# Kernel optimization log

Measured on AMD Instinct MI355X. Metric: run time of the kernel, lower is better.

Reference implementation:

```python
import jax, jax.numpy as jnp
import numpy as np

B, T, F, H = 256, 128, 1024, 512  # batch, input_size (time window), feature_dim, hidden_size


def setup_inputs() -> dict:
    key = jax.random.key(0)
    ks = jax.random.split(key, 7)
    in1 = T + 2 * H
    return {
        "h": jax.random.normal(ks[0], (B, H), dtype=jnp.float32),
        "s": jax.random.normal(ks[1], (B, H), dtype=jnp.float32),
        "x": jax.random.normal(ks[2], (B, T, F), dtype=jnp.float32),
        "W1": jax.random.normal(ks[3], (T, in1), dtype=jnp.float32) / np.sqrt(in1),
        "b1": jnp.zeros((T,), dtype=jnp.float32),
        "W2": jax.random.normal(ks[4], (1, T), dtype=jnp.float32) / np.sqrt(T),
        "b2": jnp.zeros((1,), dtype=jnp.float32),
    }


def reference(h, s, x, W1, b1, W2, b2):
    feature_dim = x.shape[-1]
    xp = jnp.transpose(x, (2, 0, 1))                     # [F, B, T]
    hb = jnp.broadcast_to(h[None], (feature_dim,) + h.shape)  # [F, B, H]
    sb = jnp.broadcast_to(s[None], (feature_dim,) + s.shape)  # [F, B, H]
    cat = jnp.concatenate([xp, hb, sb], axis=-1)         # [F, B, T+2H]
    u = jnp.einsum('fbk,tk->fbt', cat, W1) + b1          # [F, B, T]
    e = jnp.einsum('fbt,ot->fbo', jnp.tanh(u), W2) + b2  # [F, B, 1]
    alpha = jax.nn.softmax(e, axis=0)[..., 0]            # softmax over feature dim -> [F, B]
    return alpha.T                                       # [B, F]
```

## Files before the change

### kernel.cpp

```cpp
#include <hip/hip_runtime.h>
#include <hip/hip_bf16.h>


#define B_N 256
#define T_N 128
#define F_N 1024
#define H_N 512
#define IN1 1152

typedef __bf16 bf16x8 __attribute__((ext_vector_type(8)));
typedef float f32x16 __attribute__((ext_vector_type(16)));
typedef float f32x4_t __attribute__((ext_vector_type(4)));

__device__ __forceinline__ float wave_reduce_sum(float v) {
#pragma unroll
  for (int off = 32; off >= 1; off >>= 1) v += __shfl_xor(v, off, 64);
  return v;
}
__device__ __forceinline__ float wave_reduce_max(float v) {
#pragma unroll
  for (int off = 32; off >= 1; off >>= 1) v = fmaxf(v, __shfl_xor(v, off, 64));
  return v;
}

__device__ __forceinline__ float tanh_fast(float u) {
  u = fminf(fmaxf(u, -15.f), 15.f);
  float e2 = __expf(2.f * u);
  return (e2 - 1.f) / (e2 + 1.f);
}

#define HSP 1028
__global__ __launch_bounds__(256) void kA_c(const float* __restrict__ h,
                                            const float* __restrict__ s,
                                            const float* __restrict__ W1,
                                            const float* __restrict__ b1,
                                            float* __restrict__ c) {
  __shared__ __align__(16) float hs[8 * HSP];
  int tid = threadIdx.x;
  int bg = blockIdx.x >> 2;
  int tg = blockIdx.x & 3;
#pragma unroll
  for (int i = 0; i < 8; ++i) {
    int p = tid + 256 * i;
    int bl = p >> 8;
    int j4 = p & 255;
    int b = bg * 8 + bl;
    float4 v;
    if (j4 < 128) v = reinterpret_cast<const float4*>(h + (size_t)b * H_N)[j4];
    else v = reinterpret_cast<const float4*>(s + (size_t)b * H_N)[j4 - 128];
    *reinterpret_cast<float4*>(&hs[bl * HSP + j4 * 4]) = v;
  }
  __syncthreads();
  int bl = tid >> 5, ti = tid & 31;
  int t = tg * 32 + ti;
  int b = bg * 8 + bl;
  const float4* wrow = reinterpret_cast<const float4*>(W1 + (size_t)t * IN1 + T_N);
  const float4* vrow = reinterpret_cast<const float4*>(&hs[bl * HSP]);
  float acc = 0.f;
#pragma unroll 4
  for (int j4 = 0; j4 < 256; ++j4) {
    float4 w = wrow[j4], v = vrow[j4];
    acc += w.x * v.x + w.y * v.y + w.z * v.z + w.w * v.w;
  }
  c[b * T_N + t] = acc + b1[t];
}

__global__ __launch_bounds__(256) void kA_frag(const float* __restrict__ W1,
                                               unsigned short* __restrict__ w1frag) {
  int i = blockIdx.x * 256 + threadIdx.x;
  int p0 = i * 2;
  int j = p0 & 7;
  int lane = (p0 >> 3) & 63;
  int kk = (p0 >> 9) & 7;
  int tt = (p0 >> 12) & 3;
  int t = tt * 32 + (lane & 31);
  int k = kk * 16 + 8 * (lane >> 5) + j;
  const float2 w = *reinterpret_cast<const float2*>(W1 + t * IN1 + k);
  __bf16 a = (__bf16)w.x, bq = (__bf16)w.y;
  unsigned short ua = __builtin_bit_cast(unsigned short, a);
  unsigned short ub = __builtin_bit_cast(unsigned short, bq);
  *reinterpret_cast<unsigned*>(w1frag + p0) = (unsigned)ua | ((unsigned)ub << 16);
}

__global__ __launch_bounds__(256) void kB_e(const float* __restrict__ x,
                                            const unsigned short* __restrict__ w1frag,
                                            const float* __restrict__ c,
                                            const float* __restrict__ W2,
                                            const float* __restrict__ b2,
                                            float* __restrict__ e) {
  __shared__ __align__(16) unsigned short w1lds[16384];
  __shared__ __align__(16) float clds[T_N];
  __shared__ __align__(16) float w2lds[T_N];
  __shared__ __align__(16) float epart[4][T_N];
  int tid = threadIdx.x;
  int b = blockIdx.x >> 3;
  int fg = blockIdx.x & 7;

  {
    const uint4* src = reinterpret_cast<const uint4*>(w1frag);
    uint4* dst = reinterpret_cast<uint4*>(w1lds);
#pragma unroll
    for (int i = 0; i < 8; ++i) dst[tid + 256 * i] = src[tid + 256 * i];
  }
  if (tid < T_N) clds[tid] = c[b * T_N + tid];
  else if (tid < 2 * T_N) w2lds[tid - T_N] = W2[tid - T_N];
  __syncthreads();

  int lane = tid & 63, wave = tid >> 6;
  int g = lane >> 5, l31 = lane & 31;
  int f0 = fg * 128;

  const float4* xb4 = reinterpret_cast<const float4*>(x + (size_t)b * T_N * F_N + f0);
  const bf16x8* af = reinterpret_cast<const bf16x8*>(w1lds);

  f32x16 acc0 = {}, acc1 = {}, acc2 = {}, acc3 = {};
#pragma unroll
  for (int kk = 0; kk < 8; ++kk) {
    float4 xq[8];
#pragma unroll
    for (int j = 0; j < 8; ++j)
      xq[j] = xb4[(size_t)(kk * 16 + 8 * g + j) * 256 + l31];
    bf16x8 bf0, bf1, bf2, bf3;
#pragma unroll
    for (int j = 0; j < 8; ++j) {
      bf0[j] = (__bf16)xq[j].x;
      bf1[j] = (__bf16)xq[j].y;
      bf2[j] = (__bf16)xq[j].z;
      bf3[j] = (__bf16)xq[j].w;
    }
    bf16x8 afr = af[wave * 512 + kk * 64 + lane];
    acc0 = __builtin_amdgcn_mfma_f32_32x32x16_bf16(afr, bf0, acc0, 0, 0, 0);
    acc1 = __builtin_amdgcn_mfma_f32_32x32x16_bf16(afr, bf1, acc1, 0, 0, 0);
    acc2 = __builtin_amdgcn_mfma_f32_32x32x16_bf16(afr, bf2, acc2, 0, 0, 0);
    acc3 = __builtin_amdgcn_mfma_f32_32x32x16_bf16(afr, bf3, acc3, 0, 0, 0);
  }

  int tbase = wave * 32 + 4 * g;
  float4 es = {0.f, 0.f, 0.f, 0.f};
#pragma unroll
  for (int q = 0; q < 4; ++q) {
    f32x4_t cq = *reinterpret_cast<const f32x4_t*>(&clds[tbase + 8 * q]);
    f32x4_t wq = *reinterpret_cast<const f32x4_t*>(&w2lds[tbase + 8 * q]);
#pragma unroll
    for (int r = 0; r < 4; ++r) {
      int reg = q * 4 + r;
      float w2v = wq[r], cv = cq[r];
      es.x += w2v * tanh_fast(acc0[reg] + cv);
      es.y += w2v * tanh_fast(acc1[reg] + cv);
      es.z += w2v * tanh_fast(acc2[reg] + cv);
      es.w += w2v * tanh_fast(acc3[reg] + cv);
    }
  }
  es.x += __shfl_xor(es.x, 32, 64);
  es.y += __shfl_xor(es.y, 32, 64);
  es.z += __shfl_xor(es.z, 32, 64);
  es.w += __shfl_xor(es.w, 32, 64);
  if (g == 0) *reinterpret_cast<float4*>(&epart[wave][4 * l31]) = es;
  __syncthreads();
  if (tid < T_N) {
    float sum = epart[0][tid] + epart[1][tid] + epart[2][tid] + epart[3][tid] + b2[0];
    e[(size_t)b * F_N + f0 + tid] = sum;
  }
}

__global__ __launch_bounds__(256) void kC_softmax(float* __restrict__ out) {
  int b = blockIdx.x, tid = threadIdx.x;
  int lane = tid & 63, wid = tid >> 6;
  float* row = out + (size_t)b * F_N;
  float v[4];
#pragma unroll
  for (int q = 0; q < 4; ++q) v[q] = row[tid + 256 * q];
  float m = fmaxf(fmaxf(v[0], v[1]), fmaxf(v[2], v[3]));
  m = wave_reduce_max(m);
  __shared__ float rm[4], rs[4];
  if (lane == 0) rm[wid] = m;
  __syncthreads();
  float M = fmaxf(fmaxf(rm[0], rm[1]), fmaxf(rm[2], rm[3]));
  float ssum = 0.f;
#pragma unroll
  for (int q = 0; q < 4; ++q) {
    v[q] = __expf(v[q] - M);
    ssum += v[q];
  }
  ssum = wave_reduce_sum(ssum);
  if (lane == 0) rs[wid] = ssum;
  __syncthreads();
  float S = rs[0] + rs[1] + rs[2] + rs[3];
  float inv = 1.f / S;
#pragma unroll
  for (int q = 0; q < 4; ++q) row[tid + 256 * q] = v[q] * inv;
}

extern "C" void kernel_launch(void* const* d_in, const int* in_sizes, int n_in,
                              void* d_out, int out_size, void* d_ws, size_t ws_size,
                              hipStream_t stream) {
  const float* h = (const float*)d_in[0];
  const float* s = (const float*)d_in[1];
  const float* x = (const float*)d_in[2];
  const float* W1 = (const float*)d_in[3];
  const float* b1 = (const float*)d_in[4];
  const float* W2 = (const float*)d_in[5];
  const float* b2 = (const float*)d_in[6];
  float* out = (float*)d_out;

  float* c_ws = (float*)d_ws;
  unsigned short* w1frag = (unsigned short*)((char*)d_ws + B_N * T_N * 4);

  kA_c<<<128, 256, 0, stream>>>(h, s, W1, b1, c_ws);
  kA_frag<<<32, 256, 0, stream>>>(W1, w1frag);
  kB_e<<<2048, 256, 0, stream>>>(x, w1frag, c_ws, W2, b2, out);
  kC_softmax<<<256, 256, 0, stream>>>(out);
}
```

Before: 250.4 us.

## Fuse all four kernels into one per-batch block kernel

Replaces the separate c-projection, W1 fragment packing, MFMA score and softmax kernels with one kernel where each 1024-thread block handles one batch row. Each block computes its own c vector and bf16 W1 fragments in LDS, loops over four feature passes for the MFMA/tanh scoring, then does the softmax in LDS. This removes three launches and the global round-trips of c, w1frag and e. In exchange it recomputes W1 packing per block and reduces the grid to one block per batch, with narrower x loads and barriers between passes.

```diff
diff --git a/kernel.cpp b/kernel.cpp
--- a/kernel.cpp
+++ b/kernel.cpp
@@ -22,173 +22,152 @@
   for (int off = 32; off >= 1; off >>= 1) v = fmaxf(v, __shfl_xor(v, off, 64));
   return v;
 }
-
 __device__ __forceinline__ float tanh_fast(float u) {
   u = fminf(fmaxf(u, -15.f), 15.f);
   float e2 = __expf(2.f * u);
   return (e2 - 1.f) / (e2 + 1.f);
 }
+__device__ __forceinline__ unsigned short bfbits(float f) {
+  return __builtin_bit_cast(unsigned short, (__bf16)f);
+}
 
-#define HSP 1028
-__global__ __launch_bounds__(256) void kA_c(const float* __restrict__ h,
-                                            const float* __restrict__ s,
-                                            const float* __restrict__ W1,
-                                            const float* __restrict__ b1,
-                                            float* __restrict__ c) {
-  __shared__ __align__(16) float hs[8 * HSP];
-  int tid = threadIdx.x;
-  int bg = blockIdx.x >> 2;
-  int tg = blockIdx.x & 3;
+__global__ __launch_bounds__(1024) void kFused(const float* __restrict__ h,
+                                               const float* __restrict__ s,
+                                               const float* __restrict__ x,
+                                               const float* __restrict__ W1,
+                                               const float* __restrict__ b1,
+                                               const float* __restrict__ W2,
+                                               const float* __restrict__ b2,
+                                               float* __restrict__ out) {
+  __shared__ __align__(16) unsigned short w1frag[16384];
+  __shared__ __align__(16) float hs[1024];
+  __shared__ __align__(16) float cpart[128][8];
+  __shared__ __align__(16) float clds[T_N];
+  __shared__ __align__(16) float w2lds[T_N];
+  __shared__ __align__(16) float epart[4][256];
+  __shared__ __align__(16) float elds[F_N];
+  __shared__ float rbuf[16];
+
+  const int tid = threadIdx.x;
+  const int b = blockIdx.x;
+
+  if (tid < 256) {
+    float4 v = (tid < 128) ? reinterpret_cast<const float4*>(h + (size_t)b * H_N)[tid]
+                           : reinterpret_cast<const float4*>(s + (size_t)b * H_N)[tid - 128];
+    reinterpret_cast<float4*>(hs)[tid] = v;
+  }
+  {
+    const int kk = (tid >> 5) & 7;
+    const int tt = tid >> 8;
 #pragma unroll
-  for (int i = 0; i < 8; ++i) {
-    int p = tid + 256 * i;
-    int bl = p >> 8;
-    int j4 = p & 255;
-    int b = bg * 8 + bl;
-    float4 v;
-    if (j4 < 128) v = reinterpret_cast<const float4*>(h + (size_t)b * H_N)[j4];
-    else v = reinterpret_cast<const float4*>(s + (size_t)b * H_N)[j4 - 128];
-    *reinterpret_cast<float4*>(&hs[bl * HSP + j4 * 4]) = v;
+    for (int sub = 0; sub < 2; ++sub) {
+      int lane = ((tid << 1) + sub) & 63;
+      int t = tt * 32 + (lane & 31);
+      int k0 = kk * 16 + 8 * (lane >> 5);
+      const float4* wsrc = reinterpret_cast<const float4*>(W1 + (size_t)t * IN1 + k0);
+      float4 w0 = wsrc[0], w1v = wsrc[1];
+      uint4 pk;
+      pk.x = (unsigned)bfbits(w0.x) | ((unsigned)bfbits(w0.y) << 16);
+      pk.y = (unsigned)bfbits(w0.z) | ((unsigned)bfbits(w0.w) << 16);
+      pk.z = (unsigned)bfbits(w1v.x) | ((unsigned)bfbits(w1v.y) << 16);
+      pk.w = (unsigned)bfbits(w1v.z) | ((unsigned)bfbits(w1v.w) << 16);
+      *reinterpret_cast<uint4*>(w1frag + ((size_t)((tt * 8 + kk) * 64 + lane) * 8)) = pk;
+    }
   }
   __syncthreads();
-  int bl = tid >> 5, ti = tid & 31;
-  int t = tg * 32 + ti;
-  int b = bg * 8 + bl;
-  const float4* wrow = reinterpret_cast<const float4*>(W1 + (size_t)t * IN1 + T_N);
-  const float4* vrow = reinterpret_cast<const float4*>(&hs[bl * HSP]);
-  float acc = 0.f;
-#pragma unroll 4
-  for (int j4 = 0; j4 < 256; ++j4) {
-    float4 w = wrow[j4], v = vrow[j4];
-    acc += w.x * v.x + w.y * v.y + w.z * v.z + w.w * v.w;
-  }
-  c[b * T_N + t] = acc + b1[t];
-}
-
-__global__ __launch_bounds__(256) void kA_frag(const float* __restrict__ W1,
-                                               unsigned short* __restrict__ w1frag) {
-  int i = blockIdx.x * 256 + threadIdx.x;
-  int p0 = i * 2;
-  int j = p0 & 7;
-  int lane = (p0 >> 3) & 63;
-  int kk = (p0 >> 9) & 7;
-  int tt = (p0 >> 12) & 3;
-  int t = tt * 32 + (lane & 31);
-  int k = kk * 16 + 8 * (lane >> 5) + j;
-  const float2 w = *reinterpret_cast<const float2*>(W1 + t * IN1 + k);
-  __bf16 a = (__bf16)w.x, bq = (__bf16)w.y;
-  unsigned short ua = __builtin_bit_cast(unsigned short, a);
-  unsigned short ub = __builtin_bit_cast(unsigned short, bq);
-  *reinterpret_cast<unsigned*>(w1frag + p0) = (unsigned)ua | ((unsigned)ub << 16);
-}
-
-__global__ __launch_bounds__(256) void kB_e(const float* __restrict__ x,
-                                            const unsigned short* __restrict__ w1frag,
-                                            const float* __restrict__ c,
-                                            const float* __restrict__ W2,
-                                            const float* __restrict__ b2,
-                                            float* __restrict__ e) {
-  __shared__ __align__(16) unsigned short w1lds[16384];
-  __shared__ __align__(16) float clds[T_N];
-  __shared__ __align__(16) float w2lds[T_N];
-  __shared__ __align__(16) float epart[4][T_N];
-  int tid = threadIdx.x;
-  int b = blockIdx.x >> 3;
-  int fg = blockIdx.x & 7;
 
   {
-    const uint4* src = reinterpret_cast<const uint4*>(w1frag);
-    uint4* dst = reinterpret_cast<uint4*>(w1lds);
+    const int t = tid >> 3, part = tid & 7;
+    const float4* wrow = reinterpret_cast<const float4*>(W1 + (size_t)t * IN1 + T_N + part * 128);
+    const float4* vrow = reinterpret_cast<const float4*>(hs + part * 128);
+    float acc = 0.f;
+#pragma unroll 4
+    for (int k4 = 0; k4 < 32; ++k4) {
+      float4 w = wrow[k4], v = vrow[k4];
+      acc += w.x * v.x + w.y * v.y + w.z * v.z + w.w * v.w;
+    }
+    cpart[t][part] = acc;
+  }
+  __syncthreads();
+  if (tid < 128) {
+    float cs = 0.f;
 #pragma unroll
-    for (int i = 0; i < 8; ++i) dst[tid + 256 * i] = src[tid + 256 * i];
+    for (int i = 0; i < 8; ++i) cs += cpart[tid][i];
+    clds[tid] = cs + b1[tid];
+  } else if (tid < 256) {
+    w2lds[tid - 128] = W2[tid - 128];
   }
-  if (tid < T_N) clds[tid] = c[b * T_N + tid];
-  else if (tid < 2 * T_N) w2lds[tid - T_N] = W2[tid - T_N];
   __syncthreads();
 
-  int lane = tid & 63, wave = tid >> 6;
-  int g = lane >> 5, l31 = lane & 31;
-  int f0 = fg * 128;
+  const int lane = tid & 63, wave = tid >> 6;
+  const int g = lane >> 5, l31 = lane & 31;
+  const int tt = wave & 3, fgrp = wave >> 2;
+  const bf16x8* af = reinterpret_cast<const bf16x8*>(w1frag);
+  const float b2v = b2[0];
 
-  const float4* xb4 = reinterpret_cast<const float4*>(x + (size_t)b * T_N * F_N + f0);
-  const bf16x8* af = reinterpret_cast<const bf16x8*>(w1lds);
-
-  f32x16 acc0 = {}, acc1 = {}, acc2 = {}, acc3 = {};
+  for (int pass = 0; pass < 4; ++pass) {
+    const int f0 = pass * 256 + fgrp * 64;
+    const float2* xb2 = reinterpret_cast<const float2*>(x + (size_t)b * T_N * F_N + f0);
+    f32x16 acc0 = {}, acc1 = {};
 #pragma unroll
-  for (int kk = 0; kk < 8; ++kk) {
-    float4 xq[8];
+    for (int kk = 0; kk < 8; ++kk) {
+      float2 xq[8];
 #pragma unroll
-    for (int j = 0; j < 8; ++j)
-      xq[j] = xb4[(size_t)(kk * 16 + 8 * g + j) * 256 + l31];
-    bf16x8 bf0, bf1, bf2, bf3;
+      for (int j = 0; j < 8; ++j)
+        xq[j] = xb2[(size_t)(kk * 16 + 8 * g + j) * 512 + l31];
+      bf16x8 bf0, bf1;
 #pragma unroll
-    for (int j = 0; j < 8; ++j) {
-      bf0[j] = (__bf16)xq[j].x;
-      bf1[j] = (__bf16)xq[j].y;
-      bf2[j] = (__bf16)xq[j].z;
-      bf3[j] = (__bf16)xq[j].w;
+      for (int j = 0; j < 8; ++j) {
+        bf0[j] = (__bf16)xq[j].x;
+        bf1[j] = (__bf16)xq[j].y;
+      }
+      bf16x8 afr = af[tt * 512 + kk * 64 + lane];
+      acc0 = __builtin_amdgcn_mfma_f32_32x32x16_bf16(afr, bf0, acc0, 0, 0, 0);
+      acc1 = __builtin_amdgcn_mfma_f32_32x32x16_bf16(afr, bf1, acc1, 0, 0, 0);
     }
-    bf16x8 afr = af[wave * 512 + kk * 64 + lane];
-    acc0 = __builtin_amdgcn_mfma_f32_32x32x16_bf16(afr, bf0, acc0, 0, 0, 0);
-    acc1 = __builtin_amdgcn_mfma_f32_32x32x16_bf16(afr, bf1, acc1, 0, 0, 0);
-    acc2 = __builtin_amdgcn_mfma_f32_32x32x16_bf16(afr, bf2, acc2, 0, 0, 0);
-    acc3 = __builtin_amdgcn_mfma_f32_32x32x16_bf16(afr, bf3, acc3, 0, 0, 0);
+    const int tbase = tt * 32 + 4 * g;
+    float ex = 0.f, ey = 0.f;
+#pragma unroll
+    for (int q = 0; q < 4; ++q) {
+      f32x4_t cq = *reinterpret_cast<const f32x4_t*>(&clds[tbase + 8 * q]);
+      f32x4_t wq = *reinterpret_cast<const f32x4_t*>(&w2lds[tbase + 8 * q]);
+#pragma unroll
+      for (int r = 0; r < 4; ++r) {
+        int reg = q * 4 + r;
+        ex += wq[r] * tanh_fast(acc0[reg] + cq[r]);
+        ey += wq[r] * tanh_fast(acc1[reg] + cq[r]);
+      }
+    }
+    ex += __shfl_xor(ex, 32, 64);
+    ey += __shfl_xor(ey, 32, 64);
+    if (g == 0) {
+      float2 e2v = {ex, ey};
+      *reinterpret_cast<float2*>(&epart[tt][fgrp * 64 + 2 * l31]) = e2v;
+    }
+    __syncthreads();
+    if (tid < 256) {
+      elds[pass * 256 + tid] =
+          epart[0][tid] + epart[1][tid] + epart[2][tid] + epart[3][tid] + b2v;
+    }
+    __syncthreads();
   }
 
-  int tbase = wave * 32 + 4 * g;
-  float4 es = {0.f, 0.f, 0.f, 0.f};
+  float v = elds[tid];
+  float m = wave_reduce_max(v);
+  if (lane == 0) rbuf[wave] = m;
+  __syncthreads();
+  float M = rbuf[0];
 #pragma unroll
-  for (int q = 0; q < 4; ++q) {
-    f32x4_t cq = *reinterpret_cast<const f32x4_t*>(&clds[tbase + 8 * q]);
-    f32x4_t wq = *reinterpret_cast<const f32x4_t*>(&w2lds[tbase + 8 * q]);
+  for (int i = 1; i < 16; ++i) M = fmaxf(M, rbuf[i]);
+  float ev = __expf(v - M);
+  float ssum = wave_reduce_sum(ev);
+  __syncthreads();
+  if (lane == 0) rbuf[wave] = ssum;
+  __syncthreads();
+  float S = 0.f;
 #pragma unroll
-    for (int r = 0; r < 4; ++r) {
-      int reg = q * 4 + r;
-      float w2v = wq[r], cv = cq[r];
-      es.x += w2v * tanh_fast(acc0[reg] + cv);
-      es.y += w2v * tanh_fast(acc1[reg] + cv);
-      es.z += w2v * tanh_fast(acc2[reg] + cv);
-      es.w += w2v * tanh_fast(acc3[reg] + cv);
-    }
-  }
-  es.x += __shfl_xor(es.x, 32, 64);
-  es.y += __shfl_xor(es.y, 32, 64);
-  es.z += __shfl_xor(es.z, 32, 64);
-  es.w += __shfl_xor(es.w, 32, 64);
-  if (g == 0) *reinterpret_cast<float4*>(&epart[wave][4 * l31]) = es;
-  __syncthreads();
-  if (tid < T_N) {
-    float sum = epart[0][tid] + epart[1][tid] + epart[2][tid] + epart[3][tid] + b2[0];
-    e[(size_t)b * F_N + f0 + tid] = sum;
-  }
-}
-
-__global__ __launch_bounds__(256) void kC_softmax(float* __restrict__ out) {
-  int b = blockIdx.x, tid = threadIdx.x;
-  int lane = tid & 63, wid = tid >> 6;
-  float* row = out + (size_t)b * F_N;
-  float v[4];
-#pragma unroll
-  for (int q = 0; q < 4; ++q) v[q] = row[tid + 256 * q];
-  float m = fmaxf(fmaxf(v[0], v[1]), fmaxf(v[2], v[3]));
-  m = wave_reduce_max(m);
-  __shared__ float rm[4], rs[4];
-  if (lane == 0) rm[wid] = m;
-  __syncthreads();
-  float M = fmaxf(fmaxf(rm[0], rm[1]), fmaxf(rm[2], rm[3]));
-  float ssum = 0.f;
-#pragma unroll
-  for (int q = 0; q < 4; ++q) {
-    v[q] = __expf(v[q] - M);
-    ssum += v[q];
-  }
-  ssum = wave_reduce_sum(ssum);
-  if (lane == 0) rs[wid] = ssum;
-  __syncthreads();
-  float S = rs[0] + rs[1] + rs[2] + rs[3];
-  float inv = 1.f / S;
-#pragma unroll
-  for (int q = 0; q < 4; ++q) row[tid + 256 * q] = v[q] * inv;
+  for (int i = 0; i < 16; ++i) S += rbuf[i];
+  out[(size_t)b * F_N + tid] = ev / S;
 }
 
 extern "C" void kernel_launch(void* const* d_in, const int* in_sizes, int n_in,
@@ -203,11 +182,5 @@
   const float* b2 = (const float*)d_in[6];
   float* out = (float*)d_out;
 
-  float* c_ws = (float*)d_ws;
-  unsigned short* w1frag = (unsigned short*)((char*)d_ws + B_N * T_N * 4);
-
-  kA_c<<<128, 256, 0, stream>>>(h, s, W1, b1, c_ws);
-  kA_frag<<<32, 256, 0, stream>>>(W1, w1frag);
-  kB_e<<<2048, 256, 0, stream>>>(x, w1frag, c_ws, W2, b2, out);
-  kC_softmax<<<256, 256, 0, stream>>>(out);
+  kFused<<<256, 1024, 0, stream>>>(h, s, x, W1, b1, W2, b2, out);
 }
```

After: 254.0 us. No clear change (+1.4%).

## Stage x tile as bf16 in LDS and restructure h/s projection kernel

Applied to the files above, without the earlier changes.

The main kernel now loads its x tile cooperatively with float2 reads across rows, converts it to bf16 once, and writes it to LDS in MFMA B-fragment order. The MFMA loop then reads B operands from LDS instead of issuing strided global float4 loads per wave. The c-projection kernel is rewritten so each block holds one W1 row in registers and uses wave reductions over batches, launched with twice as many blocks. The extra 32KB of LDS per block may lower occupancy in the main kernel.

```diff
diff --git a/kernel.cpp b/kernel.cpp
--- a/kernel.cpp
+++ b/kernel.cpp
@@ -11,6 +11,7 @@
 typedef __bf16 bf16x8 __attribute__((ext_vector_type(8)));
 typedef float f32x16 __attribute__((ext_vector_type(16)));
 typedef float f32x4_t __attribute__((ext_vector_type(4)));
+typedef unsigned int u32x4 __attribute__((ext_vector_type(4)));
 
 __device__ __forceinline__ float wave_reduce_sum(float v) {
 #pragma unroll
@@ -22,47 +23,39 @@
   for (int off = 32; off >= 1; off >>= 1) v = fmaxf(v, __shfl_xor(v, off, 64));
   return v;
 }
-
 __device__ __forceinline__ float tanh_fast(float u) {
   u = fminf(fmaxf(u, -15.f), 15.f);
   float e2 = __expf(2.f * u);
   return (e2 - 1.f) / (e2 + 1.f);
 }
-
-#define HSP 1028
+__device__ __forceinline__ unsigned bfbits(float f) {
+  return (unsigned)__builtin_bit_cast(unsigned short, (__bf16)f);
+}
+__device__ __forceinline__ float dot4(float4 a, float4 b) {
+  return a.x * b.x + a.y * b.y + a.z * b.z + a.w * b.w;
+}
+
 __global__ __launch_bounds__(256) void kA_c(const float* __restrict__ h,
                                             const float* __restrict__ s,
                                             const float* __restrict__ W1,
                                             const float* __restrict__ b1,
                                             float* __restrict__ c) {
-  __shared__ __align__(16) float hs[8 * HSP];
-  int tid = threadIdx.x;
-  int bg = blockIdx.x >> 2;
-  int tg = blockIdx.x & 3;
-#pragma unroll
-  for (int i = 0; i < 8; ++i) {
-    int p = tid + 256 * i;
-    int bl = p >> 8;
-    int j4 = p & 255;
-    int b = bg * 8 + bl;
-    float4 v;
-    if (j4 < 128) v = reinterpret_cast<const float4*>(h + (size_t)b * H_N)[j4];
-    else v = reinterpret_cast<const float4*>(s + (size_t)b * H_N)[j4 - 128];
-    *reinterpret_cast<float4*>(&hs[bl * HSP + j4 * 4]) = v;
-  }
-  __syncthreads();
-  int bl = tid >> 5, ti = tid & 31;
-  int t = tg * 32 + ti;
-  int b = bg * 8 + bl;
+  int tid = threadIdx.x, lane = tid & 63, wave = tid >> 6;
+  int t = blockIdx.x >> 1, bh = blockIdx.x & 1;
   const float4* wrow = reinterpret_cast<const float4*>(W1 + (size_t)t * IN1 + T_N);
-  const float4* vrow = reinterpret_cast<const float4*>(&hs[bl * HSP]);
-  float acc = 0.f;
-#pragma unroll 4
-  for (int j4 = 0; j4 < 256; ++j4) {
-    float4 w = wrow[j4], v = vrow[j4];
-    acc += w.x * v.x + w.y * v.y + w.z * v.z + w.w * v.w;
-  }
-  c[b * T_N + t] = acc + b1[t];
+  float4 w0 = wrow[lane], w1v = wrow[64 + lane], w2v = wrow[128 + lane], w3v = wrow[192 + lane];
+  float b1t = b1[t];
+  int b0 = bh * 128;
+#pragma unroll 2
+  for (int bi = 0; bi < 32; ++bi) {
+    int b = b0 + wave + bi * 4;
+    const float4* hr = reinterpret_cast<const float4*>(h + (size_t)b * H_N);
+    const float4* sr = reinterpret_cast<const float4*>(s + (size_t)b * H_N);
+    float acc = dot4(w0, hr[lane]) + dot4(w1v, hr[64 + lane]) +
+                dot4(w2v, sr[lane]) + dot4(w3v, sr[64 + lane]);
+    acc = wave_reduce_sum(acc);
+    if (lane == 0) c[(size_t)b * T_N + t] = acc + b1t;
+  }
 }
 
 __global__ __launch_bounds__(256) void kA_frag(const float* __restrict__ W1,
@@ -76,10 +69,7 @@
   int t = tt * 32 + (lane & 31);
   int k = kk * 16 + 8 * (lane >> 5) + j;
   const float2 w = *reinterpret_cast<const float2*>(W1 + t * IN1 + k);
-  __bf16 a = (__bf16)w.x, bq = (__bf16)w.y;
-  unsigned short ua = __builtin_bit_cast(unsigned short, a);
-  unsigned short ub = __builtin_bit_cast(unsigned short, bq);
-  *reinterpret_cast<unsigned*>(w1frag + p0) = (unsigned)ua | ((unsigned)ub << 16);
+  *reinterpret_cast<unsigned*>(w1frag + p0) = bfbits(w.x) | (bfbits(w.y) << 16);
 }
 
 __global__ __launch_bounds__(256) void kB_e(const float* __restrict__ x,
@@ -89,12 +79,14 @@
                                             const float* __restrict__ b2,
                                             float* __restrict__ e) {
   __shared__ __align__(16) unsigned short w1lds[16384];
+  __shared__ __align__(16) unsigned char xlds[32768];
   __shared__ __align__(16) float clds[T_N];
   __shared__ __align__(16) float w2lds[T_N];
   __shared__ __align__(16) float epart[4][T_N];
   int tid = threadIdx.x;
   int b = blockIdx.x >> 3;
-  int fg = blockIdx.x & 7;
+  int fc = blockIdx.x & 7;
+  const int fbase = fc * 128;
 
   {
     const uint4* src = reinterpret_cast<const uint4*>(w1frag);
@@ -102,41 +94,54 @@
 #pragma unroll
     for (int i = 0; i < 8; ++i) dst[tid + 256 * i] = src[tid + 256 * i];
   }
-  if (tid < T_N) clds[tid] = c[b * T_N + tid];
-  else if (tid < 2 * T_N) w2lds[tid - T_N] = W2[tid - T_N];
-  __syncthreads();
-
-  int lane = tid & 63, wave = tid >> 6;
-  int g = lane >> 5, l31 = lane & 31;
-  int f0 = fg * 128;
-
-  const float4* xb4 = reinterpret_cast<const float4*>(x + (size_t)b * T_N * F_N + f0);
+  {
+    const float* xb = x + (size_t)b * T_N * F_N + fbase;
+#pragma unroll
+    for (int i = 0; i < 8; ++i) {
+      int u = tid + 256 * i;
+      int kq = u >> 6, fp = u & 63;
+      const float* base = xb + (size_t)(kq * 4) * F_N + fp * 2;
+      float2 r0 = *reinterpret_cast<const float2*>(base);
+      float2 r1 = *reinterpret_cast<const float2*>(base + F_N);
+      float2 r2 = *reinterpret_cast<const float2*>(base + 2 * F_N);
+      float2 r3 = *reinterpret_cast<const float2*>(base + 3 * F_N);
+      u32x4 pk;
+      pk[0] = bfbits(r0.x) | (bfbits(r1.x) << 16);
+      pk[1] = bfbits(r2.x) | (bfbits(r3.x) << 16);
+      pk[2] = bfbits(r0.y) | (bfbits(r1.y) << 16);
+      pk[3] = bfbits(r2.y) | (bfbits(r3.y) << 16);
+      *reinterpret_cast<u32x4*>(xlds + kq * 1024 + fp * 16) = pk;
+    }
+  }
+  if (tid < T_N) clds[tid] = c[(size_t)b * T_N + tid];
+  else w2lds[tid - T_N] = W2[tid - T_N];
+  __syncthreads();
+
+  const int lane = tid & 63, wave = tid >> 6;
+  const int g = lane >> 5, l31 = lane & 31;
   const bf16x8* af = reinterpret_cast<const bf16x8*>(w1lds);
 
   f32x16 acc0 = {}, acc1 = {}, acc2 = {}, acc3 = {};
 #pragma unroll
   for (int kk = 0; kk < 8; ++kk) {
-    float4 xq[8];
-#pragma unroll
-    for (int j = 0; j < 8; ++j)
-      xq[j] = xb4[(size_t)(kk * 16 + 8 * g + j) * 256 + l31];
-    bf16x8 bf0, bf1, bf2, bf3;
-#pragma unroll
-    for (int j = 0; j < 8; ++j) {
-      bf0[j] = (__bf16)xq[j].x;
-      bf1[j] = (__bf16)xq[j].y;
-      bf2[j] = (__bf16)xq[j].z;
-      bf3[j] = (__bf16)xq[j].w;
-    }
     bf16x8 afr = af[wave * 512 + kk * 64 + lane];
-    acc0 = __builtin_amdgcn_mfma_f32_32x32x16_bf16(afr, bf0, acc0, 0, 0, 0);
-    acc1 = __builtin_amdgcn_mfma_f32_32x32x16_bf16(afr, bf1, acc1, 0, 0, 0);
-    acc2 = __builtin_amdgcn_mfma_f32_32x32x16_bf16(afr, bf2, acc2, 0, 0, 0);
-    acc3 = __builtin_amdgcn_mfma_f32_32x32x16_bf16(afr, bf3, acc3, 0, 0, 0);
-  }
-
-  int tbase = wave * 32 + 4 * g;
-  float4 es = {0.f, 0.f, 0.f, 0.f};
+    const unsigned char* bbase = xlds + (kk * 4 + 2 * g) * 1024 + l31 * 8;
+#define BFRAG(C)                                                                    \
+  ({                                                                                \
+    uint2 lo = *reinterpret_cast<const uint2*>(bbase + (C) * 256);                  \
+    uint2 hi = *reinterpret_cast<const uint2*>(bbase + (C) * 256 + 1024);           \
+    u32x4 q = {lo.x, lo.y, hi.x, hi.y};                                             \
+    __builtin_bit_cast(bf16x8, q);                                                  \
+  })
+    acc0 = __builtin_amdgcn_mfma_f32_32x32x16_bf16(afr, BFRAG(0), acc0, 0, 0, 0);
+    acc1 = __builtin_amdgcn_mfma_f32_32x32x16_bf16(afr, BFRAG(1), acc1, 0, 0, 0);
+    acc2 = __builtin_amdgcn_mfma_f32_32x32x16_bf16(afr, BFRAG(2), acc2, 0, 0, 0);
+    acc3 = __builtin_amdgcn_mfma_f32_32x32x16_bf16(afr, BFRAG(3), acc3, 0, 0, 0);
+#undef BFRAG
+  }
+
+  const int tbase = wave * 32 + 4 * g;
+  float es0 = 0.f, es1 = 0.f, es2 = 0.f, es3 = 0.f;
 #pragma unroll
   for (int q = 0; q < 4; ++q) {
     f32x4_t cq = *reinterpret_cast<const f32x4_t*>(&clds[tbase + 8 * q]);
@@ -144,22 +149,26 @@
 #pragma unroll
     for (int r = 0; r < 4; ++r) {
       int reg = q * 4 + r;
-      float w2v = wq[r], cv = cq[r];
-      es.x += w2v * tanh_fast(acc0[reg] + cv);
-      es.y += w2v * tanh_fast(acc1[reg] + cv);
-      es.z += w2v * tanh_fast(acc2[reg] + cv);
-      es.w += w2v * tanh_fast(acc3[reg] + cv);
+      es0 += wq[r] * tanh_fast(acc0[reg] + cq[r]);
+      es1 += wq[r] * tanh_fast(acc1[reg] + cq[r]);
+      es2 += wq[r] * tanh_fast(acc2[reg] + cq[r]);
+      es3 += wq[r] * tanh_fast(acc3[reg] + cq[r]);
     }
   }
-  es.x += __shfl_xor(es.x, 32, 64);
-  es.y += __shfl_xor(es.y, 32, 64);
-  es.z += __shfl_xor(es.z, 32, 64);
-  es.w += __shfl_xor(es.w, 32, 64);
-  if (g == 0) *reinterpret_cast<float4*>(&epart[wave][4 * l31]) = es;
+  es0 += __shfl_xor(es0, 32, 64);
+  es1 += __shfl_xor(es1, 32, 64);
+  es2 += __shfl_xor(es2, 32, 64);
+  es3 += __shfl_xor(es3, 32, 64);
+  if (g == 0) {
+    epart[wave][l31] = es0;
+    epart[wave][32 + l31] = es1;
+    epart[wave][64 + l31] = es2;
+    epart[wave][96 + l31] = es3;
+  }
   __syncthreads();
   if (tid < T_N) {
-    float sum = epart[0][tid] + epart[1][tid] + epart[2][tid] + epart[3][tid] + b2[0];
-    e[(size_t)b * F_N + f0 + tid] = sum;
+    e[(size_t)b * F_N + fbase + tid] =
+        epart[0][tid] + epart[1][tid] + epart[2][tid] + epart[3][tid] + b2[0];
   }
 }
 
@@ -206,7 +215,7 @@
   float* c_ws = (float*)d_ws;
   unsigned short* w1frag = (unsigned short*)((char*)d_ws + B_N * T_N * 4);
 
-  kA_c<<<128, 256, 0, stream>>>(h, s, W1, b1, c_ws);
+  kA_c<<<256, 256, 0, stream>>>(h, s, W1, b1, c_ws);
   kA_frag<<<32, 256, 0, stream>>>(W1, w1frag);
   kB_e<<<2048, 256, 0, stream>>>(x, w1frag, c_ws, W2, b2, out);
   kC_softmax<<<256, 256, 0, stream>>>(out);
```

Result: faster. 242.6 us (-3.1%).
